# Optimization experiments

Hardware: AMD Instinct MI355X
Metric: run time of the kernel (lower is better)

The kernel has to match this reference:

```python
import jax, jax.numpy as jnp
import numpy as np

START_TAG = 7
STOP_TAG = 8
NEG = -10000.0  # matches torch.full((1,K), -10000.) in the original


def setup_inputs() -> dict:
    key = jax.random.key(0)
    k1, k2, k3, k4 = jax.random.split(key, 4)
    B, T, K = 1024, 2048, 9  # K = output_dim + 2 (START/STOP hardcoded as 7/8)
    feats = jax.random.normal(k1, (B, T, K), dtype=jnp.float32)
    tags = jax.random.randint(k2, (B, T), 0, 7)            # valid labels 0..6
    lengths = jax.random.randint(k3, (B,), 1, T + 1)        # per-sentence lengths >= 1
    transitions = jax.random.normal(k4, (K, K), dtype=jnp.float32)
    transitions = transitions.at[START_TAG, :].set(NEG)     # never transition into START
    transitions = transitions.at[:, STOP_TAG].set(NEG)      # never transition out of STOP
    return {"feats": feats, "transitions": transitions, "tags": tags, "lengths": lengths}


def _crf_nll(feats, transitions, tags, lengths):
    # feats: [B,T,K] emissions, transitions[j,i] = score of i -> j
    B, T, K = feats.shape

    def fwd_one(feat, length):
        # CRF forward algorithm (log partition), vectorized over tags,
        # lax.scan over time; masked past `length` to emulate feats[:x_len].
        alpha0 = jnp.full((K,), NEG, feat.dtype).at[START_TAG].set(0.0)

        def step(alpha, inp):
            t, f = inp
            # alpha_new[j] = logsumexp_i(alpha[i] + transitions[j,i]) + feat[t,j]
            new = jax.nn.logsumexp(alpha[None, :] + transitions, axis=1) + f
            return jnp.where(t < length, new, alpha), None

        alpha, _ = jax.lax.scan(step, alpha0, (jnp.arange(T), feat))
        return jax.nn.logsumexp(alpha + transitions[STOP_TAG])

    fwd_scores = jax.vmap(fwd_one)(feats, lengths)  # [B]

    def gold_one(feat, tg, length):
        # _score_sentence: sum_t trans[tags[t], tags[t-1]] + feat[t, tags[t]]
        prev = jnp.concatenate([jnp.array([START_TAG], tg.dtype), tg[:-1]])
        step_scores = transitions[tg, prev] + jnp.take_along_axis(feat, tg[:, None], axis=1)[:, 0]
        mask = jnp.arange(tg.shape[0]) < length
        last = tg[length - 1]
        return jnp.sum(jnp.where(mask, step_scores, 0.0)) + transitions[STOP_TAG, last]

    gold_scores = jax.vmap(gold_one)(feats, tags, lengths)  # [B]

    # neg_log_likelihood accumulates (forward - gold) per sentence, then / n
    return jnp.mean(fwd_scores - gold_scores)


def reference(feats, transitions, tags, lengths):
    return _crf_nll(feats, transitions, tags, lengths)
```

## Files before the change

kernel.cpp:

```cpp
#include <hip/hip_runtime.h>


#define START_TAG 7
#define STOP_TAG  8
#define KDIM      9
#define NS        7
#define CHUNKS    64
#define NEGINF    (-1e30f)

__device__ __forceinline__ float rfl(float x) {
    return __int_as_float(__builtin_amdgcn_readfirstlane(__float_as_int(x)));
}

__global__ __launch_bounds__(512, 4) void crf_fused_kernel(
    const float* __restrict__ feats,
    const float* __restrict__ trans,
    const int*   __restrict__ tags,
    const int*   __restrict__ lengths,
    float* __restrict__ out,
    int B, int T)
{
    __shared__ float s_trans[81];
    __shared__ float s_E[49];
    __shared__ float s_M[CHUNKS * 64];
    __shared__ float s_gold[8];

    const int tid = threadIdx.x;
    const int b   = blockIdx.x;

    if (tid < 81) s_trans[tid] = trans[tid];
    if (tid >= 128 && tid < 177) {
        int k = tid - 128;
        s_E[k] = __expf(trans[(k / 7) * 9 + (k % 7)]);
    }
    __syncthreads();

    const int    len   = lengths[b];
    const int*   tg    = tags  + (size_t)b * T;
    const float* fbase = feats + (size_t)b * T * KDIM;
    const int    Lb    = (len > 1) ? ((len - 1 + CHUNKS - 1) / CHUNKS) : 1;

    {
        int per = T >> 9; if (per < 1) per = 1;
        int t0  = tid * per;
        float g = 0.f;
        if (t0 < len) {
            int te   = min(t0 + per, len);
            int prev = (t0 == 0) ? START_TAG : tg[t0 - 1];
            if (per == 4) {
                #pragma unroll
                for (int k = 0; k < 4; ++k) {
                    int t   = t0 + k;
                    int tc  = min(t, te - 1);
                    int cur = tg[tc];
                    float v = s_trans[cur * 9 + prev] + fbase[(size_t)tc * KDIM + cur];
                    g += (t < te) ? v : 0.f;
                    prev = cur;
                }
            } else {
                for (int k = 0; k < per; ++k) {
                    int t   = t0 + k;
                    int tc  = min(t, te - 1);
                    int cur = tg[tc];
                    float v = s_trans[cur * 9 + prev] + fbase[(size_t)tc * KDIM + cur];
                    g += (t < te) ? v : 0.f;
                    prev = cur;
                }
            }
            if (len - 1 >= t0 && len - 1 < t0 + per)
                g += s_trans[STOP_TAG * 9 + tg[len - 1]];
        }
        #pragma unroll
        for (int off = 32; off > 0; off >>= 1) g += __shfl_xor(g, off, 64);
        if ((tid & 63) == 0) s_gold[tid >> 6] = g;
    }

    {
        const int lane8  = tid & 7;
        const int c      = tid >> 3;
        const int tstart = 1 + c * Lb;
        const int tend   = min(tstart + Lb, len);

        if (lane8 < NS) {
            float* Mw = s_M + c * 64;
            if (tstart < tend) {
                float E[49];
                #pragma unroll
                for (int k = 0; k < 49; ++k) E[k] = rfl(s_E[k]);

                int baddr[NS];
                #pragma unroll
                for (int j = 0; j < NS; ++j) baddr[j] = (((tid & 56) | j) << 2);

                float p[NS];
                #pragma unroll
                for (int j = 0; j < NS; ++j) p[j] = (j == lane8) ? 1.f : 0.f;
                float s = 0.f;
                int rem = tend - tstart;

                const float* fp = fbase + (size_t)tstart * KDIM + lane8;

                #define CRF_MAT(EF) do {                                        \
                    float q[NS];                                                \
                    _Pragma("unroll")                                           \
                    for (int j = 0; j < NS; ++j) {                              \
                        float acc = E[j * 7] * p[0];                            \
                        _Pragma("unroll")                                       \
                        for (int i = 1; i < NS; ++i)                            \
                            acc = fmaf(E[j * 7 + i], p[i], acc);                \
                        q[j] = acc;                                             \
                    }                                                           \
                    _Pragma("unroll")                                           \
                    for (int j = 0; j < NS; ++j) p[j] = q[j] * EF[j];           \
                } while (0)

                #define CRF_BCAST(DST, XF) do {                                 \
                    float _e = __expf(XF);                                      \
                    _Pragma("unroll")                                           \
                    for (int j = 0; j < NS; ++j)                                \
                        DST[j] = __int_as_float(                                \
                            __builtin_amdgcn_ds_bpermute(                       \
                                baddr[j], __float_as_int(_e)));                 \
                } while (0)

                #define CRF_STEP(XF) do {                                       \
                    float _ef[NS];                                              \
                    CRF_BCAST(_ef, XF);                                         \
                    CRF_MAT(_ef);                                               \
                } while (0)

                #define CRF_RENORM() do {                                       \
                    float m = p[0];                                             \
                    _Pragma("unroll")                                           \
                    for (int j = 1; j < NS; ++j) m = fmaxf(m, p[j]);            \
                    float rm = __builtin_amdgcn_rcpf(m);                        \
                    _Pragma("unroll")                                           \
                    for (int j = 0; j < NS; ++j) p[j] *= rm;                    \
                    s += __logf(m);                                             \
                } while (0)

                int o1 = KDIM * min(1, rem - 1);
                int o2 = KDIM * min(2, rem - 1);
                int o3 = KDIM * min(3, rem - 1);
                float x0 = fp[0], x1 = fp[o1], x2 = fp[o2], x3 = fp[o3];
                fp += 4 * KDIM;

                while (rem >= 8) {
                    float y0 = fp[0], y1 = fp[KDIM], y2 = fp[2 * KDIM], y3 = fp[3 * KDIM];
                    fp += 4 * KDIM;
                    float efA[NS], efB[NS], efC[NS], efD[NS];
                    CRF_BCAST(efA, x0);
                    CRF_BCAST(efB, x1);
                    CRF_BCAST(efC, x2);
                    CRF_BCAST(efD, x3);
                    CRF_MAT(efA); CRF_MAT(efB); CRF_MAT(efC); CRF_MAT(efD);
                    CRF_RENORM();
                    x0 = y0; x1 = y1; x2 = y2; x3 = y3;
                    rem -= 4;
                }
                if (rem > 4) {
                    int e1 = KDIM * min(1, rem - 5);
                    int e2 = KDIM * min(2, rem - 5);
                    float y0 = fp[0], y1 = fp[e1], y2 = fp[e2];
                    float efA[NS], efB[NS], efC[NS], efD[NS];
                    CRF_BCAST(efA, x0);
                    CRF_BCAST(efB, x1);
                    CRF_BCAST(efC, x2);
                    CRF_BCAST(efD, x3);
                    CRF_MAT(efA); CRF_MAT(efB); CRF_MAT(efC); CRF_MAT(efD);
                    CRF_RENORM();
                    x0 = y0; x1 = y1; x2 = y2;
                    rem -= 4;
                }
                CRF_STEP(x0);
                if (rem > 1) CRF_STEP(x1);
                if (rem > 2) CRF_STEP(x2);
                if (rem > 3) CRF_STEP(x3);

                #pragma unroll
                for (int j = 0; j < NS; ++j)
                    Mw[j * 8 + lane8] = __logf(p[j]) + s;

                #undef CRF_MAT
                #undef CRF_BCAST
                #undef CRF_STEP
                #undef CRF_RENORM
            } else {
                #pragma unroll
                for (int j = 0; j < NS; ++j)
                    Mw[j * 8 + lane8] = (j == lane8) ? 0.f : NEGINF;
            }
        }
    }
    __syncthreads();

    {
        const int l = tid & 63;
        const int w = tid >> 6;
        const int i = l & 7;
        float* seg = s_M + w * 512;

        float A = seg[l];
        int baddr[NS];
        #pragma unroll
        for (int k = 0; k < NS; ++k) baddr[k] = ((k << 3) | i) << 2;

        #pragma unroll
        for (int c = 1; c < 8; ++c) {
            const float* Mr = seg + c * 64 + (l & 56);
            float4 r0 = *(const float4*)(Mr);
            float4 r1 = *(const float4*)(Mr + 4);
            float ac[NS];
            #pragma unroll
            for (int k = 0; k < NS; ++k)
                ac[k] = __int_as_float(__builtin_amdgcn_ds_bpermute(
                            baddr[k], __float_as_int(A)));
            float t0 = r0.x + ac[0], t1 = r0.y + ac[1], t2 = r0.z + ac[2];
            float t3 = r0.w + ac[3], t4 = r1.x + ac[4], t5 = r1.y + ac[5];
            float t6 = r1.z + ac[6];
            float tm = fmaxf(fmaxf(fmaxf(t0, t1), fmaxf(t2, t3)),
                             fmaxf(fmaxf(t4, t5), t6));
            float sum = ((__expf(t0 - tm) + __expf(t1 - tm)) +
                         (__expf(t2 - tm) + __expf(t3 - tm))) +
                        ((__expf(t4 - tm) + __expf(t5 - tm)) + __expf(t6 - tm));
            A = tm + __logf(sum);
        }
        seg[l] = A;
    }
    __syncthreads();

    if (tid < 8) {
        const int  lane  = tid;
        const bool isrow = (lane < NS);
        const int  row   = isrow ? lane : 0;

        float a[NS];
        #pragma unroll
        for (int i = 0; i < NS; ++i)
            a[i] = s_trans[i * 9 + START_TAG] + fbase[i];
        float S;
        {
            float mm = fmaxf(fmaxf(fmaxf(a[0], a[1]), fmaxf(a[2], a[3])),
                             fmaxf(fmaxf(a[4], a[5]), a[6]));
            S = mm;
            #pragma unroll
            for (int i = 0; i < NS; ++i) a[i] -= mm;
        }

        const float* Mr0 = s_M + row * 8;
        float4 mA = *(const float4*)(Mr0);
        float4 mB = *(const float4*)(Mr0 + 4);
        #pragma unroll
        for (int w = 0; w < 8; ++w) {
            int wn = min(w + 1, 7);
            float4 nA = *(const float4*)(Mr0 + wn * 512);
            float4 nB = *(const float4*)(Mr0 + wn * 512 + 4);
            float t0 = mA.x + a[0], t1 = mA.y + a[1], t2 = mA.z + a[2];
            float t3 = mA.w + a[3], t4 = mB.x + a[4], t5 = mB.y + a[5];
            float t6 = mB.z + a[6];
            float tm = fmaxf(fmaxf(fmaxf(t0, t1), fmaxf(t2, t3)),
                             fmaxf(fmaxf(t4, t5), t6));
            float e0 = __expf(t0 - tm), e1 = __expf(t1 - tm), e2 = __expf(t2 - tm);
            float e3 = __expf(t3 - tm), e4 = __expf(t4 - tm), e5 = __expf(t5 - tm);
            float e6 = __expf(t6 - tm);
            float sum = ((e0 + e1) + (e2 + e3)) + ((e4 + e5) + e6);
            float na = isrow ? (tm + __logf(sum)) : NEGINF;
            float b0 = __shfl(na, 0, 8), b1 = __shfl(na, 1, 8), b2 = __shfl(na, 2, 8);
            float b3 = __shfl(na, 3, 8), b4 = __shfl(na, 4, 8), b5 = __shfl(na, 5, 8);
            float b6 = __shfl(na, 6, 8);
            float mm = fmaxf(fmaxf(fmaxf(b0, b1), fmaxf(b2, b3)),
                             fmaxf(fmaxf(b4, b5), b6));
            a[0] = b0 - mm; a[1] = b1 - mm; a[2] = b2 - mm;
            a[3] = b3 - mm; a[4] = b4 - mm; a[5] = b5 - mm;
            a[6] = b6 - mm;
            S += mm;
            mA = nA; mB = nB;
        }

        if (lane == 0) {
            float t0 = a[0] + s_trans[STOP_TAG * 9 + 0];
            float t1 = a[1] + s_trans[STOP_TAG * 9 + 1];
            float t2 = a[2] + s_trans[STOP_TAG * 9 + 2];
            float t3 = a[3] + s_trans[STOP_TAG * 9 + 3];
            float t4 = a[4] + s_trans[STOP_TAG * 9 + 4];
            float t5 = a[5] + s_trans[STOP_TAG * 9 + 5];
            float t6 = a[6] + s_trans[STOP_TAG * 9 + 6];
            float tm = fmaxf(fmaxf(fmaxf(t0, t1), fmaxf(t2, t3)),
                             fmaxf(fmaxf(t4, t5), t6));
            float sum = ((__expf(t0 - tm) + __expf(t1 - tm)) +
                         (__expf(t2 - tm) + __expf(t3 - tm))) +
                        ((__expf(t4 - tm) + __expf(t5 - tm)) + __expf(t6 - tm));
            float fwd = S + tm + __logf(sum);
            float g = (s_gold[0] + s_gold[1] + s_gold[2] + s_gold[3]) +
                      (s_gold[4] + s_gold[5] + s_gold[6] + s_gold[7]);
            atomicAdd(out, (fwd - g) * (1.0f / (float)B));
        }
    }
}

__global__ void init_out_kernel(float* out) {
    if (threadIdx.x == 0) out[0] = 0.f;
}

extern "C" void kernel_launch(void* const* d_in, const int* in_sizes, int n_in,
                              void* d_out, int out_size, void* d_ws, size_t ws_size,
                              hipStream_t stream) {
    const float* feats   = (const float*)d_in[0];
    const float* trans   = (const float*)d_in[1];
    const int*   tags    = (const int*)d_in[2];
    const int*   lengths = (const int*)d_in[3];

    int B = in_sizes[3];
    int T = in_sizes[2] / B;

    init_out_kernel<<<1, 64, 0, stream>>>((float*)d_out);
    crf_fused_kernel<<<B, 512, 0, stream>>>(
        feats, trans, tags, lengths, (float*)d_out, B, T);
}
```

Baseline: 142.4 us.

## Split CRF into per-wavefront chunk kernel and separate fold/gold kernel

The single fused 512-thread block per sentence becomes two kernels. The first runs 256-thread blocks in which each wavefront handles one slice of 8 chunks for one sentence, reduces them within the wavefront using only an LDS waitcnt instead of a block barrier, and writes the slice result to workspace. The second kernel reads the slice matrices per sentence, computes the gold score and performs the final fold. This removes block-wide syncs and should improve occupancy and scheduling flexibility, at the cost of an extra launch and a workspace round trip through global memory.

```diff
diff --git a/kernel.cpp b/kernel.cpp
--- a/kernel.cpp
+++ b/kernel.cpp
@@ -5,88 +5,50 @@
 #define STOP_TAG  8
 #define KDIM      9
 #define NS        7
-#define CHUNKS    64
+#define CPS       64
+#define SLICES    8
 #define NEGINF    (-1e30f)
 
 __device__ __forceinline__ float rfl(float x) {
     return __int_as_float(__builtin_amdgcn_readfirstlane(__float_as_int(x)));
 }
 
-__global__ __launch_bounds__(512, 4) void crf_fused_kernel(
+__global__ __launch_bounds__(256, 8) void crf_chunk_kernel(
     const float* __restrict__ feats,
     const float* __restrict__ trans,
-    const int*   __restrict__ tags,
     const int*   __restrict__ lengths,
-    float* __restrict__ out,
+    float* __restrict__ g_seg,
     int B, int T)
 {
-    __shared__ float s_trans[81];
     __shared__ float s_E[49];
-    __shared__ float s_M[CHUNKS * 64];
-    __shared__ float s_gold[8];
+    __shared__ float s_M[4 * 512];
 
     const int tid = threadIdx.x;
-    const int b   = blockIdx.x;
-
-    if (tid < 81) s_trans[tid] = trans[tid];
-    if (tid >= 128 && tid < 177) {
-        int k = tid - 128;
-        s_E[k] = __expf(trans[(k / 7) * 9 + (k % 7)]);
-    }
+    if (tid < 49) s_E[tid] = __expf(trans[(tid / 7) * 9 + (tid % 7)]);
     __syncthreads();
 
+    const int widx = tid >> 6;
+    const int W    = blockIdx.x * 4 + widx;
+    const int s    = W / B;
+    const int b    = W - s * B;
+
     const int    len   = lengths[b];
-    const int*   tg    = tags  + (size_t)b * T;
     const float* fbase = feats + (size_t)b * T * KDIM;
-    const int    Lb    = (len > 1) ? ((len - 1 + CHUNKS - 1) / CHUNKS) : 1;
-
-    {
-        int per = T >> 9; if (per < 1) per = 1;
-        int t0  = tid * per;
-        float g = 0.f;
-        if (t0 < len) {
-            int te   = min(t0 + per, len);
-            int prev = (t0 == 0) ? START_TAG : tg[t0 - 1];
-            if (per == 4) {
-                #pragma unroll
-                for (int k = 0; k < 4; ++k) {
-                    int t   = t0 + k;
-                    int tc  = min(t, te - 1);
-                    int cur = tg[tc];
-                    float v = s_trans[cur * 9 + prev] + fbase[(size_t)tc * KDIM + cur];
-                    g += (t < te) ? v : 0.f;
-                    prev = cur;
-                }
-            } else {
-                for (int k = 0; k < per; ++k) {
-                    int t   = t0 + k;
-                    int tc  = min(t, te - 1);
-                    int cur = tg[tc];
-                    float v = s_trans[cur * 9 + prev] + fbase[(size_t)tc * KDIM + cur];
-                    g += (t < te) ? v : 0.f;
-                    prev = cur;
-                }
-            }
-            if (len - 1 >= t0 && len - 1 < t0 + per)
-                g += s_trans[STOP_TAG * 9 + tg[len - 1]];
-        }
-        #pragma unroll
-        for (int off = 32; off > 0; off >>= 1) g += __shfl_xor(g, off, 64);
-        if ((tid & 63) == 0) s_gold[tid >> 6] = g;
-    }
+    const int    Lb    = (len > 1) ? ((len - 1 + CPS - 1) / CPS) : 1;
 
     {
         const int lane8  = tid & 7;
-        const int c      = tid >> 3;
+        const int k      = (tid >> 3) & 7;
+        const int c      = s * 8 + k;
         const int tstart = 1 + c * Lb;
         const int tend   = min(tstart + Lb, len);
 
         if (lane8 < NS) {
-            float* Mw = s_M + c * 64;
+            float* Mw = s_M + widx * 512 + k * 64;
             if (tstart < tend) {
                 float E[49];
                 #pragma unroll
-                for (int k = 0; k < 49; ++k) E[k] = rfl(s_E[k]);
+                for (int e = 0; e < 49; ++e) E[e] = rfl(s_E[e]);
 
                 int baddr[NS];
                 #pragma unroll
@@ -95,7 +57,7 @@
                 float p[NS];
                 #pragma unroll
                 for (int j = 0; j < NS; ++j) p[j] = (j == lane8) ? 1.f : 0.f;
-                float s = 0.f;
+                float sc = 0.f;
                 int rem = tend - tstart;
 
                 const float* fp = fbase + (size_t)tstart * KDIM + lane8;
@@ -136,7 +98,7 @@
                     float rm = __builtin_amdgcn_rcpf(m);                        \
                     _Pragma("unroll")                                           \
                     for (int j = 0; j < NS; ++j) p[j] *= rm;                    \
-                    s += __logf(m);                                             \
+                    sc += __logf(m);                                            \
                 } while (0)
 
                 int o1 = KDIM * min(1, rem - 1);
@@ -179,7 +141,7 @@
 
                 #pragma unroll
                 for (int j = 0; j < NS; ++j)
-                    Mw[j * 8 + lane8] = __logf(p[j]) + s;
+                    Mw[j * 8 + lane8] = __logf(p[j]) + sc;
 
                 #undef CRF_MAT
                 #undef CRF_BCAST
@@ -192,22 +154,22 @@
             }
         }
     }
-    __syncthreads();
+
+    asm volatile("s_waitcnt lgkmcnt(0)" ::: "memory");
 
     {
-        const int l = tid & 63;
-        const int w = tid >> 6;
-        const int i = l & 7;
-        float* seg = s_M + w * 512;
-
-        float A = seg[l];
+        const int l  = tid & 63;
+        const int i  = l & 7;
+        float* sg = s_M + widx * 512;
+
+        float A = sg[l];
         int baddr[NS];
         #pragma unroll
         for (int k = 0; k < NS; ++k) baddr[k] = ((k << 3) | i) << 2;
 
         #pragma unroll
         for (int c = 1; c < 8; ++c) {
-            const float* Mr = seg + c * 64 + (l & 56);
+            const float* Mr = sg + c * 64 + (l & 56);
             float4 r0 = *(const float4*)(Mr);
             float4 r1 = *(const float4*)(Mr + 4);
             float ac[NS];
@@ -225,7 +187,71 @@
                         ((__expf(t4 - tm) + __expf(t5 - tm)) + __expf(t6 - tm));
             A = tm + __logf(sum);
         }
-        seg[l] = A;
+        g_seg[((size_t)(b * SLICES + s)) * 64 + l] = A;
+    }
+}
+
+__global__ __launch_bounds__(256) void crf_fold_kernel(
+    const float* __restrict__ feats,
+    const float* __restrict__ trans,
+    const int*   __restrict__ tags,
+    const int*   __restrict__ lengths,
+    const float* __restrict__ g_seg,
+    float* __restrict__ out,
+    int B, int T)
+{
+    __shared__ float s_trans[81];
+    __shared__ float s_S[512];
+    __shared__ float s_gold[4];
+
+    const int tid = threadIdx.x;
+    const int b   = blockIdx.x;
+
+    if (tid < 81) s_trans[tid] = trans[tid];
+    {
+        const float* sp = g_seg + (size_t)b * 512;
+        s_S[tid]       = sp[tid];
+        s_S[tid + 256] = sp[tid + 256];
+    }
+    __syncthreads();
+
+    const int    len   = lengths[b];
+    const int*   tg    = tags  + (size_t)b * T;
+    const float* fbase = feats + (size_t)b * T * KDIM;
+
+    {
+        int per = (T >> 8) > 0 ? (T >> 8) : 1;
+        int t0  = tid * per;
+        float g = 0.f;
+        if (t0 < len) {
+            int te   = min(t0 + per, len);
+            int prev = (t0 == 0) ? START_TAG : tg[t0 - 1];
+            if (per == 8) {
+                #pragma unroll
+                for (int k = 0; k < 8; ++k) {
+                    int t   = t0 + k;
+                    int tc  = min(t, te - 1);
+                    int cur = tg[tc];
+                    float v = s_trans[cur * 9 + prev] + fbase[(size_t)tc * KDIM + cur];
+                    g += (t < te) ? v : 0.f;
+                    prev = cur;
+                }
+            } else {
+                for (int k = 0; k < per; ++k) {
+                    int t   = t0 + k;
+                    int tc  = min(t, te - 1);
+                    int cur = tg[tc];
+                    float v = s_trans[cur * 9 + prev] + fbase[(size_t)tc * KDIM + cur];
+                    g += (t < te) ? v : 0.f;
+                    prev = cur;
+                }
+            }
+            if (len - 1 >= t0 && len - 1 < t0 + per)
+                g += s_trans[STOP_TAG * 9 + tg[len - 1]];
+        }
+        #pragma unroll
+        for (int off = 32; off > 0; off >>= 1) g += __shfl_xor(g, off, 64);
+        if ((tid & 63) == 0) s_gold[tid >> 6] = g;
     }
     __syncthreads();
 
@@ -247,14 +273,14 @@
             for (int i = 0; i < NS; ++i) a[i] -= mm;
         }
 
-        const float* Mr0 = s_M + row * 8;
+        const float* Mr0 = s_S + row * 8;
         float4 mA = *(const float4*)(Mr0);
         float4 mB = *(const float4*)(Mr0 + 4);
         #pragma unroll
         for (int w = 0; w < 8; ++w) {
             int wn = min(w + 1, 7);
-            float4 nA = *(const float4*)(Mr0 + wn * 512);
-            float4 nB = *(const float4*)(Mr0 + wn * 512 + 4);
+            float4 nA = *(const float4*)(Mr0 + wn * 64);
+            float4 nB = *(const float4*)(Mr0 + wn * 64 + 4);
             float t0 = mA.x + a[0], t1 = mA.y + a[1], t2 = mA.z + a[2];
             float t3 = mA.w + a[3], t4 = mB.x + a[4], t5 = mB.y + a[5];
             float t6 = mB.z + a[6];
@@ -291,8 +317,7 @@
                          (__expf(t2 - tm) + __expf(t3 - tm))) +
                         ((__expf(t4 - tm) + __expf(t5 - tm)) + __expf(t6 - tm));
             float fwd = S + tm + __logf(sum);
-            float g = (s_gold[0] + s_gold[1] + s_gold[2] + s_gold[3]) +
-                      (s_gold[4] + s_gold[5] + s_gold[6] + s_gold[7]);
+            float g = s_gold[0] + s_gold[1] + s_gold[2] + s_gold[3];
             atomicAdd(out, (fwd - g) * (1.0f / (float)B));
         }
     }
@@ -313,7 +338,11 @@
     int B = in_sizes[3];
     int T = in_sizes[2] / B;
 
+    float* seg = (float*)d_ws;
+
     init_out_kernel<<<1, 64, 0, stream>>>((float*)d_out);
-    crf_fused_kernel<<<B, 512, 0, stream>>>(
-        feats, trans, tags, lengths, (float*)d_out, B, T);
-}
+    crf_chunk_kernel<<<B * SLICES / 4, 256, 0, stream>>>(
+        feats, trans, lengths, seg, B, T);
+    crf_fold_kernel<<<B, 256, 0, stream>>>(
+        feats, trans, tags, lengths, seg, (float*)d_out, B, T);
+}
```

New measurement: 164.9 us. +15.8%, slower.

## Software-pipeline emission broadcasts ahead of matrix steps and drop block barrier

Applied to the files above, without the earlier changes.

In the CRF chunk scan, the exp and ds_bpermute broadcast for the next timestep's emissions is now issued before the current step's 7x7 matrix-vector product. A sched_barrier and s_setprio raise priority on the math so the LDS permute latency overlaps with FMA work. The __syncthreads before the chunk-combine phase becomes an LDS waitcnt, which is valid only because each wave reads back the s_M chunks it wrote itself. The change adds register pressure from the extra emission buffers, and it depends on that per-wave data ownership holding.

```diff
diff --git a/kernel.cpp b/kernel.cpp
--- a/kernel.cpp
+++ b/kernel.cpp
@@ -86,7 +86,7 @@
             if (tstart < tend) {
                 float E[49];
                 #pragma unroll
-                for (int k = 0; k < 49; ++k) E[k] = rfl(s_E[k]);
+                for (int e = 0; e < 49; ++e) E[e] = rfl(s_E[e]);
 
                 int baddr[NS];
                 #pragma unroll
@@ -123,6 +123,14 @@
                                 baddr[j], __float_as_int(_e)));                 \
                 } while (0)
 
+                #define CRF_PSTEP(EFN, XN, EFC) do {                            \
+                    CRF_BCAST(EFN, XN);                                         \
+                    __builtin_amdgcn_sched_barrier(0);                          \
+                    __builtin_amdgcn_s_setprio(1);                              \
+                    CRF_MAT(EFC);                                               \
+                    __builtin_amdgcn_s_setprio(0);                              \
+                } while (0)
+
                 #define CRF_STEP(XF) do {                                       \
                     float _ef[NS];                                              \
                     CRF_BCAST(_ef, XF);                                         \
@@ -145,16 +153,20 @@
                 float x0 = fp[0], x1 = fp[o1], x2 = fp[o2], x3 = fp[o3];
                 fp += 4 * KDIM;
 
+                float ef0[NS];
+                CRF_BCAST(ef0, x0);
+
                 while (rem >= 8) {
                     float y0 = fp[0], y1 = fp[KDIM], y2 = fp[2 * KDIM], y3 = fp[3 * KDIM];
                     fp += 4 * KDIM;
-                    float efA[NS], efB[NS], efC[NS], efD[NS];
-                    CRF_BCAST(efA, x0);
-                    CRF_BCAST(efB, x1);
-                    CRF_BCAST(efC, x2);
-                    CRF_BCAST(efD, x3);
-                    CRF_MAT(efA); CRF_MAT(efB); CRF_MAT(efC); CRF_MAT(efD);
+                    float ef1[NS], ef2[NS], ef3[NS], ef4[NS];
+                    CRF_PSTEP(ef1, x1, ef0);
+                    CRF_PSTEP(ef2, x2, ef1);
+                    CRF_PSTEP(ef3, x3, ef2);
+                    CRF_PSTEP(ef4, y0, ef3);
                     CRF_RENORM();
+                    #pragma unroll
+                    for (int j = 0; j < NS; ++j) ef0[j] = ef4[j];
                     x0 = y0; x1 = y1; x2 = y2; x3 = y3;
                     rem -= 4;
                 }
@@ -162,17 +174,18 @@
                     int e1 = KDIM * min(1, rem - 5);
                     int e2 = KDIM * min(2, rem - 5);
                     float y0 = fp[0], y1 = fp[e1], y2 = fp[e2];
-                    float efA[NS], efB[NS], efC[NS], efD[NS];
-                    CRF_BCAST(efA, x0);
-                    CRF_BCAST(efB, x1);
-                    CRF_BCAST(efC, x2);
-                    CRF_BCAST(efD, x3);
-                    CRF_MAT(efA); CRF_MAT(efB); CRF_MAT(efC); CRF_MAT(efD);
+                    float ef1[NS], ef2[NS], ef3[NS], ef4[NS];
+                    CRF_PSTEP(ef1, x1, ef0);
+                    CRF_PSTEP(ef2, x2, ef1);
+                    CRF_PSTEP(ef3, x3, ef2);
+                    CRF_PSTEP(ef4, y0, ef3);
                     CRF_RENORM();
+                    #pragma unroll
+                    for (int j = 0; j < NS; ++j) ef0[j] = ef4[j];
                     x0 = y0; x1 = y1; x2 = y2;
                     rem -= 4;
                 }
-                CRF_STEP(x0);
+                CRF_MAT(ef0);
                 if (rem > 1) CRF_STEP(x1);
                 if (rem > 2) CRF_STEP(x2);
                 if (rem > 3) CRF_STEP(x3);
@@ -183,6 +196,7 @@
 
                 #undef CRF_MAT
                 #undef CRF_BCAST
+                #undef CRF_PSTEP
                 #undef CRF_STEP
                 #undef CRF_RENORM
             } else {
@@ -192,7 +206,8 @@
             }
         }
     }
-    __syncthreads();
+
+    asm volatile("s_waitcnt lgkmcnt(0)" ::: "memory");
 
     {
         const int l = tid & 63;
```

Result: no change. 143.1 us (+0.5%).
